# Kernel tuning notes

Measured on AMD Instinct MI355X. Metric: run time of the kernel, lower is better.

Reference implementation:

```python
import jax, jax.numpy as jnp
import numpy as np

B, N, C = 2, 65536, 256
H, D, S = 8, 64, 64  # heads, dim_head, slice_num
INNER = H * D


def setup_inputs() -> dict:
    key = jax.random.key(0)
    ks = jax.random.split(key, 8)
    scale_in = 1.0 / np.sqrt(C)
    scale_d = 1.0 / np.sqrt(D)
    return {
        "x": jax.random.normal(ks[0], (B, N, C), dtype=jnp.float32),
        "W_x": jax.random.uniform(ks[1], (C, INNER), jnp.float32, -scale_in, scale_in),
        "b_x": jax.random.uniform(ks[2], (INNER,), jnp.float32, -scale_in, scale_in),
        "W_fx": jax.random.uniform(ks[3], (C, INNER), jnp.float32, -scale_in, scale_in),
        "b_fx": jax.random.uniform(ks[4], (INNER,), jnp.float32, -scale_in, scale_in),
        "W_slice": jax.random.uniform(ks[5], (D, S), jnp.float32, -scale_d, scale_d),
        "b_slice": jax.random.uniform(ks[6], (S,), jnp.float32, -scale_d, scale_d),
        "temperature": jnp.full((1, H, 1, 1), 0.5, dtype=jnp.float32),
    }


def _split_heads(t):
    # (B, N, H*D) -> (B, H, N, D)
    return t.reshape(B, N, H, D).transpose(0, 2, 1, 3)


def reference(x, W_x, b_x, W_fx, b_fx, W_slice, b_slice, temperature):
    projected_x = _split_heads(x @ W_x + b_x)          # (B,H,N,D)
    fx = _split_heads(x @ W_fx + b_fx)                 # (B,H,N,D)
    slice_proj = projected_x @ W_slice + b_slice       # (B,H,N,S)
    temp = jnp.clip(temperature, 0.5, 5.0)
    slice_weights = jax.nn.softmax(slice_proj / temp, axis=-1)  # (B,H,N,S)
    slice_norm = slice_weights.sum(axis=2)             # (B,H,S)
    normed = slice_weights / (slice_norm[:, :, None, :] + 0.01)
    # weighted token aggregation: (B,H,S,D)
    slice_tokens = jnp.einsum("bhns,bhnd->bhsd", normed, fx)
    return slice_tokens
```

## Files before the change

### kernel.cpp

```cpp
#include <hip/hip_runtime.h>

typedef _Float16 f16;
typedef __attribute__((ext_vector_type(8))) _Float16 f16x8;
typedef __attribute__((ext_vector_type(4))) _Float16 f16x4;
typedef __attribute__((ext_vector_type(4))) float    f32x4;

#define MFMA(a,b,c) __builtin_amdgcn_mfma_f32_16x16x32_f16(a,b,c,0,0,0)

constexpr int Bc = 2, Nc = 65536, Cc = 256, Hc = 8;
constexpr int CHUNK = 512;
constexpr int LDX = 72;
constexpr int LDT = 136;


__device__ __forceinline__ f32x4 splat4(float v) { f32x4 r; r.x=v; r.y=v; r.z=v; r.w=v; return r; }
__device__ __forceinline__ f16x8 pack8(float4 a, float4 b) {
  f16x8 r = { (f16)a.x,(f16)a.y,(f16)a.z,(f16)a.w,(f16)b.x,(f16)b.y,(f16)b.z,(f16)b.w };
  return r;
}

__device__ __forceinline__ void wave_bar() {
  asm volatile("s_waitcnt lgkmcnt(0)" ::: "memory");
  __builtin_amdgcn_s_barrier();
  __builtin_amdgcn_sched_barrier(0);
}

__global__ void prep_a(const float* __restrict__ Wx, const float* __restrict__ Wfx,
                       const float* __restrict__ Wsl, const float* __restrict__ bx,
                       const float* __restrict__ bsl, f16* __restrict__ WC,
                       float* __restrict__ bsp, float* __restrict__ Tz) {
  __shared__ float tile[64][72];
  const int b = blockIdx.x, t = threadIdx.x;
  if (b < 32) {
    const int k0 = (b & 3) * 64, c0 = (b >> 2) * 64;
    const int r = t >> 4, c4 = (t & 15) * 4;
    #pragma unroll
    for (int i = 0; i < 4; ++i) {
      float4 v = *(const float4*)&Wfx[(size_t)(k0 + r + i*16)*512 + c0 + c4];
      tile[r + i*16][c4] = v.x; tile[r + i*16][c4+1] = v.y;
      tile[r + i*16][c4+2] = v.z; tile[r + i*16][c4+3] = v.w;
    }
    __syncthreads();
    const int cl = t >> 2, kq = t & 3;
    const int col = c0 + cl, h = col >> 6, n = col & 63;
    f16 tmp[16];
    #pragma unroll
    for (int j = 0; j < 16; ++j) tmp[j] = (f16)tile[kq*16 + j][cl];
    f16* dst = WC + (size_t)(h*128 + n)*256 + k0 + kq*16;
    *(f16x8*)dst       = *(f16x8*)&tmp[0];
    *(f16x8*)(dst + 8) = *(f16x8*)&tmp[8];
  } else if (b < 96) {
    const int bb = b - 32;
    const int h = bb >> 3, k0 = (bb & 7) * 32;
    const int k = t & 31, sq = t >> 5;
    float accs[8];
    #pragma unroll
    for (int j = 0; j < 8; ++j) accs[j] = 0.f;
    for (int d = 0; d < 64; ++d) {
      float a = Wx[(size_t)(k0 + k)*512 + h*64 + d];
      #pragma unroll
      for (int j = 0; j < 8; ++j) accs[j] += a * Wsl[d*64 + sq*8 + j];
    }
    #pragma unroll
    for (int j = 0; j < 8; ++j)
      WC[(size_t)(h*128 + 64 + sq*8 + j)*256 + k0 + k] = (f16)accs[j];
  } else if (b == 96) {
    for (int u = t; u < 512; u += 256) {
      int h = u >> 6, s = u & 63;
      float a = bsl[s];
      for (int d = 0; d < 64; ++d) a += bx[h*64 + d] * Wsl[d*64 + s];
      bsp[h*64 + s] = a;
    }
  } else {
    float4 z; z.x = z.y = z.z = z.w = 0.f;
    ((float4*)Tz)[(b - 97) * 256 + t] = z;
  }
}

__global__ __launch_bounds__(256, 2)
void fused_main(const float* __restrict__ x,   const float* __restrict__ bfx,
                const float* __restrict__ bsp, const float* __restrict__ temp,
                const f16* __restrict__ WC,    float* __restrict__ Tg,
                float* __restrict__ normg) {
  __shared__ alignas(16) char smem[4 * 128 * LDX * 2];
  f16* X0 = (f16*)smem;
  f16* W0 = X0 + 128 * LDX;
  f16* X1 = W0 + 128 * LDX;
  f16* W1 = X1 + 128 * LDX;
  f16* sm_fxT = X1;
  f16* sm_wT  = W1;

  const int j    = blockIdx.x;
  const int xcd  = j & 7, slot = j >> 3;
  const int chunk = xcd * 32 + (slot >> 3);
  const int h     = slot & 7;

  const int tid = threadIdx.x;
  const int wv = tid >> 6, lane = tid & 63, quad = lane >> 4, ln = lane & 15;
  const int wm = wv >> 1, wn = wv & 1;
  const long tokBase = (long)chunk * CHUNK;
  const int b  = (int)(tokBase >> 16);
  const int bh = b * Hc + h;

  const float tc = fminf(fmaxf(temp[h], 0.5f), 5.0f);
  const float k2 = 1.44269504f / tc;

  float bv[4];
  {
    const float* bb = (wn == 0) ? (bfx + h*64) : (bsp + h*64);
    #pragma unroll
    for (int nt = 0; nt < 4; ++nt) bv[nt] = bb[nt*16 + ln];
  }

  f32x4 Tacc[2][2];
  #pragma unroll
  for (int i = 0; i < 2; ++i) { Tacc[i][0] = splat4(0.f); Tacc[i][1] = splat4(0.f); }
  float nacc[4] = {0.f, 0.f, 0.f, 0.f};
  const int ci = wv >> 1, cj = wv & 1;

  const f16* WCh = WC + (size_t)h * 128 * 256;

  const int r0 = tid >> 2, seg = tid & 3;
  const int wrow = tid >> 1, whalf = tid & 1;

  float4 xr[8]; f16x8 wr[4];
  auto loadx = [&](int m0, int kb) {
    const float* p = x + (tokBase + (long)m0*128 + r0)*Cc + kb*64 + seg*16;
    xr[0] = *(const float4*)p;        xr[1] = *(const float4*)(p + 4);
    xr[2] = *(const float4*)(p + 8);  xr[3] = *(const float4*)(p + 12);
    p += 64 * Cc;
    xr[4] = *(const float4*)p;        xr[5] = *(const float4*)(p + 4);
    xr[6] = *(const float4*)(p + 8);  xr[7] = *(const float4*)(p + 12);
  };
  auto loadw = [&](int kb) {
    const f16* p = WCh + wrow*256 + kb*64 + whalf*32;
    wr[0] = *(const f16x8*)p;         wr[1] = *(const f16x8*)(p + 8);
    wr[2] = *(const f16x8*)(p + 16);  wr[3] = *(const f16x8*)(p + 24);
  };

  loadx(0, 0); loadw(0);

  for (int m0 = 0; m0 < 4; ++m0) {
    f32x4 acc[4][4];
    #pragma unroll
    for (int mt = 0; mt < 4; ++mt)
      #pragma unroll
      for (int nt = 0; nt < 4; ++nt) acc[mt][nt] = splat4(bv[nt]);

    for (int kb = 0; kb < 4; ++kb) {
      const int t = m0*4 + kb;
      f16* sx = (t & 1) ? X1 : X0;
      f16* sw = (t & 1) ? W1 : W0;
      *(f16x8*)&sx[r0*LDX + seg*16]          = pack8(xr[0], xr[1]);
      *(f16x8*)&sx[r0*LDX + seg*16 + 8]      = pack8(xr[2], xr[3]);
      *(f16x8*)&sx[(r0+64)*LDX + seg*16]     = pack8(xr[4], xr[5]);
      *(f16x8*)&sx[(r0+64)*LDX + seg*16 + 8] = pack8(xr[6], xr[7]);
      *(f16x8*)&sw[wrow*LDX + whalf*32]      = wr[0];
      *(f16x8*)&sw[wrow*LDX + whalf*32 +  8] = wr[1];
      *(f16x8*)&sw[wrow*LDX + whalf*32 + 16] = wr[2];
      *(f16x8*)&sw[wrow*LDX + whalf*32 + 24] = wr[3];
      { int nt_ = t + 1;
        if (nt_ < 16) { loadx(nt_ >> 2, nt_ & 3); loadw(nt_ & 3); } }
      wave_bar();
      #pragma unroll
      for (int ks = 0; ks < 2; ++ks) {
        f16x8 af[4], bf[4];
        #pragma unroll
        for (int mt = 0; mt < 4; ++mt)
          af[mt] = *(const f16x8*)&sx[(wm*64 + mt*16 + ln)*LDX + ks*32 + quad*8];
        #pragma unroll
        for (int nt = 0; nt < 4; ++nt)
          bf[nt] = *(const f16x8*)&sw[(wn*64 + nt*16 + ln)*LDX + ks*32 + quad*8];
        #pragma unroll
        for (int mt = 0; mt < 4; ++mt)
          #pragma unroll
          for (int nt = 0; nt < 4; ++nt)
            acc[mt][nt] = MFMA(af[mt], bf[nt], acc[mt][nt]);
      }
    }
    wave_bar();

    if (wn == 0) {
      #pragma unroll
      for (int mt = 0; mt < 4; ++mt)
        #pragma unroll
        for (int nt = 0; nt < 4; ++nt) {
          f16x4 v = { (f16)acc[mt][nt][0], (f16)acc[mt][nt][1],
                      (f16)acc[mt][nt][2], (f16)acc[mt][nt][3] };
          *(f16x4*)&sm_fxT[(nt*16 + ln)*LDT + wm*64 + mt*16 + quad*4] = v;
        }
    } else {
      #pragma unroll
      for (int mt = 0; mt < 4; ++mt) {
        float e[4][4], wout[4][4];
        #pragma unroll
        for (int nt = 0; nt < 4; ++nt)
          #pragma unroll
          for (int rg = 0; rg < 4; ++rg)
            e[nt][rg] = exp2f(acc[mt][nt][rg] * k2);
        #pragma unroll
        for (int rg = 0; rg < 4; ++rg) {
          float rs = e[0][rg] + e[1][rg] + e[2][rg] + e[3][rg];
          #pragma unroll
          for (int dd = 1; dd < 16; dd <<= 1) rs += __shfl_xor(rs, dd, 64);
          float inv = 1.0f / rs;
          #pragma unroll
          for (int nt = 0; nt < 4; ++nt) {
            wout[nt][rg] = e[nt][rg] * inv;
            nacc[nt] += wout[nt][rg];
          }
        }
        #pragma unroll
        for (int nt = 0; nt < 4; ++nt) {
          f16x4 v = { (f16)wout[nt][0], (f16)wout[nt][1],
                      (f16)wout[nt][2], (f16)wout[nt][3] };
          *(f16x4*)&sm_wT[(nt*16 + ln)*LDT + wm*64 + mt*16 + quad*4] = v;
        }
      }
    }
    wave_bar();

    #pragma unroll
    for (int ks = 0; ks < 4; ++ks) {
      f16x8 a0 = *(const f16x8*)&sm_wT [(ci*32 +      ln)*LDT + ks*32 + quad*8];
      f16x8 a1 = *(const f16x8*)&sm_wT [(ci*32 + 16 + ln)*LDT + ks*32 + quad*8];
      f16x8 b0 = *(const f16x8*)&sm_fxT[(cj*32 +      ln)*LDT + ks*32 + quad*8];
      f16x8 b1 = *(const f16x8*)&sm_fxT[(cj*32 + 16 + ln)*LDT + ks*32 + quad*8];
      Tacc[0][0] = MFMA(a0, b0, Tacc[0][0]);
      Tacc[0][1] = MFMA(a0, b1, Tacc[0][1]);
      Tacc[1][0] = MFMA(a1, b0, Tacc[1][0]);
      Tacc[1][1] = MFMA(a1, b1, Tacc[1][1]);
    }
  }

  float* Tb = Tg + bh * 4096;
  #pragma unroll
  for (int mt2 = 0; mt2 < 2; ++mt2)
    #pragma unroll
    for (int nt2 = 0; nt2 < 2; ++nt2)
      #pragma unroll
      for (int rg = 0; rg < 4; ++rg) {
        int s = ci*32 + mt2*16 + quad*4 + rg;
        int d = cj*32 + nt2*16 + ln;
        atomicAdd(&Tb[s*64 + d], Tacc[mt2][nt2][rg]);
      }
  if (wn == 1) {
    #pragma unroll
    for (int nt = 0; nt < 4; ++nt) {
      float v = nacc[nt];
      v += __shfl_xor(v, 16, 64);
      v += __shfl_xor(v, 32, 64);
      if (lane < 16) atomicAdd(&normg[bh*64 + nt*16 + ln], v);
    }
  }
}

__global__ void finalize(const float* __restrict__ Tg, const float* __restrict__ normg,
                         float* __restrict__ out) {
  int i = blockIdx.x * 256 + threadIdx.x;
  out[i] = Tg[i] / (normg[i >> 6] + 0.01f);
}

extern "C" void kernel_launch(void* const* d_in, const int* in_sizes, int n_in,
                              void* d_out, int out_size, void* d_ws, size_t ws_size,
                              hipStream_t stream) {
  const float* x    = (const float*)d_in[0];
  const float* Wx   = (const float*)d_in[1];
  const float* bx   = (const float*)d_in[2];
  const float* Wfx  = (const float*)d_in[3];
  const float* bfx  = (const float*)d_in[4];
  const float* Wsl  = (const float*)d_in[5];
  const float* bsl  = (const float*)d_in[6];
  const float* temp = (const float*)d_in[7];
  float* out = (float*)d_out;

  float* Tg    = (float*)d_ws;
  float* normg = Tg + 16 * 4096;
  f16*   WC    = (f16*)((char*)d_ws + 266240);
  float* bsp   = (float*)((char*)d_ws + 790528);

  prep_a    <<<162, 256, 0, stream>>>(Wx, Wfx, Wsl, bx, bsl, WC, bsp, Tg);
  fused_main<<<2048, 256, 0, stream>>>(x, bfx, bsp, temp, WC, Tg, normg);
  finalize  <<<256, 256, 0, stream>>>(Tg, normg, out);
}
```

Measured before the change: 343.9 us.

## Pre-convert x to fp16 and stream tiles via global_load_lds DMA

```diff
diff --git a/kernel.cpp b/kernel.cpp
--- a/kernel.cpp
+++ b/kernel.cpp
@@ -12,6 +12,8 @@
 constexpr int LDX = 72;
 constexpr int LDT = 136;
 
+constexpr size_t X16_OFF = 1048576;
+constexpr size_t WS_BIG  = X16_OFF + (size_t)131072 * 256 * 2;
 
 __device__ __forceinline__ f32x4 splat4(float v) { f32x4 r; r.x=v; r.y=v; r.z=v; r.w=v; return r; }
 __device__ __forceinline__ f16x8 pack8(float4 a, float4 b) {
@@ -19,18 +21,38 @@
   return r;
 }
 
-__device__ __forceinline__ void wave_bar() {
+__device__ __forceinline__ void gl_lds16(const f16* g, f16* l) {
+  __builtin_amdgcn_global_load_lds((const __attribute__((address_space(1))) void*)g,
+                                   (__attribute__((address_space(3))) void*)l, 16, 0, 0);
+}
+__device__ __forceinline__ void bar_lgkm() {
   asm volatile("s_waitcnt lgkmcnt(0)" ::: "memory");
   __builtin_amdgcn_s_barrier();
   __builtin_amdgcn_sched_barrier(0);
 }
-
-__global__ void prep_a(const float* __restrict__ Wx, const float* __restrict__ Wfx,
-                       const float* __restrict__ Wsl, const float* __restrict__ bx,
-                       const float* __restrict__ bsl, f16* __restrict__ WC,
-                       float* __restrict__ bsp, float* __restrict__ Tz) {
+template<int N> __device__ __forceinline__ void bar_vm() {
+  __builtin_amdgcn_sched_barrier(0);
+  asm volatile("s_waitcnt vmcnt(%0)" :: "i"(N) : "memory");
+  __builtin_amdgcn_s_barrier();
+  __builtin_amdgcn_sched_barrier(0);
+}
+
+__global__ void prep_b(const float* __restrict__ x, const float* __restrict__ Wx,
+                       const float* __restrict__ Wfx, const float* __restrict__ Wsl,
+                       const float* __restrict__ bx, const float* __restrict__ bsl,
+                       f16* __restrict__ WC, float* __restrict__ bsp,
+                       float* __restrict__ Tz, f16* __restrict__ x16, int cvt_blocks) {
   __shared__ float tile[64][72];
-  const int b = blockIdx.x, t = threadIdx.x;
+  int b = blockIdx.x;
+  const int t = threadIdx.x;
+  if (b < cvt_blocks) {
+    const long i = ((long)b * 256 + t) * 8;
+    float4 a = *(const float4*)&x[i];
+    float4 c = *(const float4*)&x[i + 4];
+    *(f16x8*)&x16[i] = pack8(a, c);
+    return;
+  }
+  b -= cvt_blocks;
   if (b < 32) {
     const int k0 = (b & 3) * 64, c0 = (b >> 2) * 64;
     const int r = t >> 4, c4 = (t & 15) * 4;
@@ -45,7 +67,7 @@
     const int col = c0 + cl, h = col >> 6, n = col & 63;
     f16 tmp[16];
     #pragma unroll
-    for (int j = 0; j < 16; ++j) tmp[j] = (f16)tile[kq*16 + j][cl];
+    for (int jj = 0; jj < 16; ++jj) tmp[jj] = (f16)tile[kq*16 + jj][cl];
     f16* dst = WC + (size_t)(h*128 + n)*256 + k0 + kq*16;
     *(f16x8*)dst       = *(f16x8*)&tmp[0];
     *(f16x8*)(dst + 8) = *(f16x8*)&tmp[8];
@@ -55,15 +77,15 @@
     const int k = t & 31, sq = t >> 5;
     float accs[8];
     #pragma unroll
-    for (int j = 0; j < 8; ++j) accs[j] = 0.f;
+    for (int jj = 0; jj < 8; ++jj) accs[jj] = 0.f;
     for (int d = 0; d < 64; ++d) {
       float a = Wx[(size_t)(k0 + k)*512 + h*64 + d];
       #pragma unroll
-      for (int j = 0; j < 8; ++j) accs[j] += a * Wsl[d*64 + sq*8 + j];
-    }
-    #pragma unroll
-    for (int j = 0; j < 8; ++j)
-      WC[(size_t)(h*128 + 64 + sq*8 + j)*256 + k0 + k] = (f16)accs[j];
+      for (int jj = 0; jj < 8; ++jj) accs[jj] += a * Wsl[d*64 + sq*8 + jj];
+    }
+    #pragma unroll
+    for (int jj = 0; jj < 8; ++jj)
+      WC[(size_t)(h*128 + 64 + sq*8 + jj)*256 + k0 + k] = (f16)accs[jj];
   } else if (b == 96) {
     for (int u = t; u < 512; u += 256) {
       int h = u >> 6, s = u & 63;
@@ -77,11 +99,189 @@
   }
 }
 
+__global__ __launch_bounds__(256, 1)
+void fused_dma(const f16* __restrict__ x16, const float* __restrict__ bfx,
+               const float* __restrict__ bsp, const float* __restrict__ temp,
+               const f16* __restrict__ WC,   float* __restrict__ Tg,
+               float* __restrict__ normg) {
+  __shared__ alignas(1024) f16 smem[32768];
+  f16* X0 = smem;          f16* W0 = smem +  8192;
+  f16* X1 = smem + 16384;  f16* W1 = smem + 24576;
+  f16* sm_fxT = X1;
+  f16* sm_wT  = W1;
+
+  const int j    = blockIdx.x;
+  const int xcd  = j & 7, slot = j >> 3;
+  const int chunk = xcd * 32 + (slot >> 3);
+  const int h     = slot & 7;
+
+  const int tid = threadIdx.x;
+  const int wv = tid >> 6, lane = tid & 63, quad = lane >> 4, ln = lane & 15;
+  const int wm = wv >> 1, wn = wv & 1;
+  const long tokBase = (long)chunk * CHUNK;
+  const int b  = (int)(tokBase >> 16);
+  const int bh = b * Hc + h;
+
+  const float tc = fminf(fmaxf(temp[h], 0.5f), 5.0f);
+  const float k2 = 1.44269504f / tc;
+
+  float bv[4];
+  {
+    const float* bb = (wn == 0) ? (bfx + h*64) : (bsp + h*64);
+    #pragma unroll
+    for (int nt = 0; nt < 4; ++nt) bv[nt] = bb[nt*16 + ln];
+  }
+
+  f32x4 Tacc[2][2];
+  #pragma unroll
+  for (int i = 0; i < 2; ++i) { Tacc[i][0] = splat4(0.f); Tacc[i][1] = splat4(0.f); }
+  float nacc[4] = {0.f, 0.f, 0.f, 0.f};
+  const int ci = wv >> 1, cj = wv & 1;
+
+  const f16* WCh = WC + (size_t)h * 128 * 256;
+
+  const int l8 = lane >> 3;
+  const int sl = (lane & 7) ^ l8;
+  const f16* xg = x16 + (tokBase + wv*32 + l8) * 256 + sl*8;
+  const f16* wg = WCh + (wv*32 + l8) * 256 + sl*8;
+
+  auto stage = [&](int tt) {
+    f16* bx_ = (tt & 1) ? X1 : X0;
+    f16* bw_ = (tt & 1) ? W1 : W0;
+    const f16* gx = xg + (long)(tt >> 2) * (128*256) + (tt & 3) * 64;
+    const f16* gw = wg + (tt & 3) * 64;
+    f16* lx = bx_ + wv * 2048;
+    f16* lw = bw_ + wv * 2048;
+    #pragma unroll
+    for (int i = 0; i < 4; ++i) {
+      gl_lds16(gx + i*2048, lx + i*512);
+      gl_lds16(gw + i*2048, lw + i*512);
+    }
+  };
+
+  const int swl = (ln & 7) * 8;
+  const int swt = ln * 8;
+
+  stage(0);
+
+  for (int m0 = 0; m0 < 4; ++m0) {
+    f32x4 acc[4][4];
+    #pragma unroll
+    for (int mt = 0; mt < 4; ++mt)
+      #pragma unroll
+      for (int nt = 0; nt < 4; ++nt) acc[mt][nt] = splat4(bv[nt]);
+
+    #pragma unroll
+    for (int kb = 0; kb < 4; ++kb) {
+      const int t = m0*4 + kb;
+      if (m0 == 3 && kb == 3) { bar_vm<0>(); }
+      else                    { stage(t + 1); bar_vm<8>(); }
+      const f16* sx = (t & 1) ? X1 : X0;
+      const f16* sw = (t & 1) ? W1 : W0;
+      #pragma unroll
+      for (int ks = 0; ks < 2; ++ks) {
+        f16x8 af[4], bf[4];
+        #pragma unroll
+        for (int mt = 0; mt < 4; ++mt)
+          af[mt] = *(const f16x8*)&sx[(wm*64 + mt*16 + ln)*64 + ((ks*32 + quad*8) ^ swl)];
+        #pragma unroll
+        for (int nt = 0; nt < 4; ++nt)
+          bf[nt] = *(const f16x8*)&sw[(wn*64 + nt*16 + ln)*64 + ((ks*32 + quad*8) ^ swl)];
+        #pragma unroll
+        for (int mt = 0; mt < 4; ++mt)
+          #pragma unroll
+          for (int nt = 0; nt < 4; ++nt)
+            acc[mt][nt] = MFMA(af[mt], bf[nt], acc[mt][nt]);
+      }
+      bar_lgkm();
+    }
+
+    if (wn == 0) {
+      #pragma unroll
+      for (int mt = 0; mt < 4; ++mt)
+        #pragma unroll
+        for (int nt = 0; nt < 4; ++nt) {
+          f16x4 v = { (f16)acc[mt][nt][0], (f16)acc[mt][nt][1],
+                      (f16)acc[mt][nt][2], (f16)acc[mt][nt][3] };
+          *(f16x4*)&sm_fxT[(nt*16 + ln)*128 + ((wm*64 + mt*16 + quad*4) ^ swt)] = v;
+        }
+    } else {
+      #pragma unroll
+      for (int mt = 0; mt < 4; ++mt) {
+        float e[4][4], wout[4][4];
+        #pragma unroll
+        for (int nt = 0; nt < 4; ++nt)
+          #pragma unroll
+          for (int rg = 0; rg < 4; ++rg)
+            e[nt][rg] = exp2f(acc[mt][nt][rg] * k2);
+        #pragma unroll
+        for (int rg = 0; rg < 4; ++rg) {
+          float rs = e[0][rg] + e[1][rg] + e[2][rg] + e[3][rg];
+          #pragma unroll
+          for (int dd = 1; dd < 16; dd <<= 1) rs += __shfl_xor(rs, dd, 64);
+          float inv = 1.0f / rs;
+          #pragma unroll
+          for (int nt = 0; nt < 4; ++nt) {
+            wout[nt][rg] = e[nt][rg] * inv;
+            nacc[nt] += wout[nt][rg];
+          }
+        }
+        #pragma unroll
+        for (int nt = 0; nt < 4; ++nt) {
+          f16x4 v = { (f16)wout[nt][0], (f16)wout[nt][1],
+                      (f16)wout[nt][2], (f16)wout[nt][3] };
+          *(f16x4*)&sm_wT[(nt*16 + ln)*128 + ((wm*64 + mt*16 + quad*4) ^ swt)] = v;
+        }
+      }
+    }
+    bar_lgkm();
+
+    #pragma unroll
+    for (int ks = 0; ks < 4; ++ks) {
+      f16x8 a0 = *(const f16x8*)&sm_wT [(ci*32 +      ln)*128 + ((ks*32 + quad*8) ^ swt)];
+      f16x8 a1 = *(const f16x8*)&sm_wT [(ci*32 + 16 + ln)*128 + ((ks*32 + quad*8) ^ swt)];
+      f16x8 b0 = *(const f16x8*)&sm_fxT[(cj*32 +      ln)*128 + ((ks*32 + quad*8) ^ swt)];
+      f16x8 b1 = *(const f16x8*)&sm_fxT[(cj*32 + 16 + ln)*128 + ((ks*32 + quad*8) ^ swt)];
+      Tacc[0][0] = MFMA(a0, b0, Tacc[0][0]);
+      Tacc[0][1] = MFMA(a0, b1, Tacc[0][1]);
+      Tacc[1][0] = MFMA(a1, b0, Tacc[1][0]);
+      Tacc[1][1] = MFMA(a1, b1, Tacc[1][1]);
+    }
+    bar_lgkm();
+  }
+
+  float* Tb = Tg + bh * 4096;
+  #pragma unroll
+  for (int mt2 = 0; mt2 < 2; ++mt2)
+    #pragma unroll
+    for (int nt2 = 0; nt2 < 2; ++nt2)
+      #pragma unroll
+      for (int rg = 0; rg < 4; ++rg) {
+        int s = ci*32 + mt2*16 + quad*4 + rg;
+        int d = cj*32 + nt2*16 + ln;
+        atomicAdd(&Tb[s*64 + d], Tacc[mt2][nt2][rg]);
+      }
+  if (wn == 1) {
+    #pragma unroll
+    for (int nt = 0; nt < 4; ++nt) {
+      float v = nacc[nt];
+      v += __shfl_xor(v, 16, 64);
+      v += __shfl_xor(v, 32, 64);
+      if (lane < 16) atomicAdd(&normg[bh*64 + nt*16 + ln], v);
+    }
+  }
+}
+
+__device__ __forceinline__ void wave_bar() {
+  asm volatile("s_waitcnt lgkmcnt(0)" ::: "memory");
+  __builtin_amdgcn_s_barrier();
+  __builtin_amdgcn_sched_barrier(0);
+}
 __global__ __launch_bounds__(256, 2)
-void fused_main(const float* __restrict__ x,   const float* __restrict__ bfx,
-                const float* __restrict__ bsp, const float* __restrict__ temp,
-                const f16* __restrict__ WC,    float* __restrict__ Tg,
-                float* __restrict__ normg) {
+void fused_reg(const float* __restrict__ x,   const float* __restrict__ bfx,
+               const float* __restrict__ bsp, const float* __restrict__ temp,
+               const f16* __restrict__ WC,    float* __restrict__ Tg,
+               float* __restrict__ normg) {
   __shared__ alignas(16) char smem[4 * 128 * LDX * 2];
   f16* X0 = (f16*)smem;
   f16* W0 = X0 + 128 * LDX;
@@ -119,7 +319,6 @@
   const int ci = wv >> 1, cj = wv & 1;
 
   const f16* WCh = WC + (size_t)h * 128 * 256;
-
   const int r0 = tid >> 2, seg = tid & 3;
   const int wrow = tid >> 1, whalf = tid & 1;
 
@@ -278,8 +477,14 @@
   float* normg = Tg + 16 * 4096;
   f16*   WC    = (f16*)((char*)d_ws + 266240);
   float* bsp   = (float*)((char*)d_ws + 790528);
-
-  prep_a    <<<162, 256, 0, stream>>>(Wx, Wfx, Wsl, bx, bsl, WC, bsp, Tg);
-  fused_main<<<2048, 256, 0, stream>>>(x, bfx, bsp, temp, WC, Tg, normg);
-  finalize  <<<256, 256, 0, stream>>>(Tg, normg, out);
-}
+  f16*   x16   = (f16*)((char*)d_ws + X16_OFF);
+
+  if (ws_size >= WS_BIG) {
+    prep_b   <<<16384 + 162, 256, 0, stream>>>(x, Wx, Wfx, Wsl, bx, bsl, WC, bsp, Tg, x16, 16384);
+    fused_dma<<<2048, 256, 0, stream>>>(x16, bfx, bsp, temp, WC, Tg, normg);
+  } else {
+    prep_b   <<<162, 256, 0, stream>>>(x, Wx, Wfx, Wsl, bx, bsl, WC, bsp, Tg, x16, 0);
+    fused_reg<<<2048, 256, 0, stream>>>(x, bfx, bsp, temp, WC, Tg, normg);
+  }
+  finalize <<<256, 256, 0, stream>>>(Tg, normg, out);
+}
```

Result: slower. 411.6 us (+19.7%).
